# Optimization experiments

Measured on AMD Instinct MI355X. Metric: run time of the kernel, lower is better.

## Reference

```python
import jax, jax.numpy as jnp
import numpy as np

NODE_TYPES = ["patient", "visit", "symptom", "procedure", "disease", "drug"]
N = {"patient": 20000, "visit": 100000, "symptom": 4000, "procedure": 8000,
     "disease": 10000, "drug": 4000}
D = 128          # embedding_dim == hidden_channels
N_LAYERS = 4     # conv1..conv4
# (src, dst) per relation; reverse edges included so every node type gets messages
REL = [("patient", "visit"), ("visit", "patient"),
       ("visit", "symptom"), ("symptom", "visit"),
       ("visit", "procedure"), ("procedure", "visit"),
       ("visit", "disease"), ("disease", "visit"),
       ("visit", "drug"), ("drug", "visit")]
E_FWD = {("patient", "visit"): 100000, ("visit", "symptom"): 300000,
         ("visit", "procedure"): 200000, ("visit", "disease"): 250000,
         ("visit", "drug"): 300000}
EI_NAMES = ["ei_pv", "ei_vp", "ei_vs", "ei_sv", "ei_vpr", "ei_prv",
            "ei_vd", "ei_dv", "ei_vdr", "ei_drv"]
E_LABEL = 200000


def setup_inputs() -> dict:
    key = jax.random.key(0)
    ks = iter(jax.random.split(key, 64))
    inp = {}
    for nt in NODE_TYPES:
        inp[f"node_id_{nt}"] = jnp.arange(N[nt], dtype=jnp.int32)
        inp[f"emb_{nt}"] = jax.random.normal(next(ks), (N[nt], D), jnp.float32)
    for name, (src, dst) in zip(EI_NAMES, REL):
        e = E_FWD.get((src, dst), E_FWD.get((dst, src)))
        row = jax.random.randint(next(ks), (e,), 0, N[src], dtype=jnp.int32)
        col = jax.random.randint(next(ks), (e,), 0, N[dst], dtype=jnp.int32)
        inp[name] = jnp.stack([row, col])
    R = len(REL)
    inp["W_l"] = jax.random.normal(next(ks), (N_LAYERS, R, D, D), jnp.float32) * 0.05
    inp["b_l"] = jnp.zeros((N_LAYERS, R, D), jnp.float32)
    inp["W_r"] = jax.random.normal(next(ks), (N_LAYERS, R, D, D), jnp.float32) * 0.05
    inp["cls_w1"] = jax.random.normal(next(ks), (2 * D, D), jnp.float32) * 0.05
    inp["cls_b1"] = jnp.zeros((D,), jnp.float32)
    inp["cls_w2"] = jax.random.normal(next(ks), (D, 1), jnp.float32) * 0.05
    inp["cls_b2"] = jnp.zeros((1,), jnp.float32)
    row = jax.random.randint(next(ks), (E_LABEL,), 0, N["visit"], dtype=jnp.int32)
    col = jax.random.randint(next(ks), (E_LABEL,), 0, N["drug"], dtype=jnp.int32)
    inp["edge_label_index"] = jnp.stack([row, col])
    inp["edge_label"] = jax.random.bernoulli(next(ks), 0.5, (E_LABEL,)).astype(jnp.float32)
    return inp


def _hetero_sage_layer(x, eis, Wl, bl, Wr):
    # to_hetero semantics: out[dst] = sum over edge types (src,rel,dst) of
    #   SAGEConv_rel: lin_l(mean_j x[src][j]) + lin_r(x[dst])   (PyG defaults)
    out = {nt: jnp.zeros_like(v) for nt, v in x.items()}
    for r, (src, dst) in enumerate(REL):
        ei = eis[r]
        n_dst = x[dst].shape[0]
        msg = jax.ops.segment_sum(x[src][ei[0]], ei[1], num_segments=n_dst)
        deg = jax.ops.segment_sum(jnp.ones((ei.shape[1],), x[src].dtype), ei[1],
                                  num_segments=n_dst)
        mean = msg / jnp.maximum(deg, 1.0)[:, None]  # empty segments stay 0 as in PyG
        out[dst] = out[dst] + mean @ Wl[r] + bl[r] + x[dst] @ Wr[r]
    return out


def reference(node_id_patient, node_id_visit, node_id_symptom, node_id_procedure,
              node_id_disease, node_id_drug,
              emb_patient, emb_visit, emb_symptom, emb_procedure, emb_disease, emb_drug,
              ei_pv, ei_vp, ei_vs, ei_sv, ei_vpr, ei_prv, ei_vd, ei_dv, ei_vdr, ei_drv,
              W_l, b_l, W_r, cls_w1, cls_b1, cls_w2, cls_b2,
              edge_label_index, edge_label):
    x = {"patient": emb_patient[node_id_patient],
         "visit": emb_visit[node_id_visit],
         "symptom": emb_symptom[node_id_symptom],
         "procedure": emb_procedure[node_id_procedure],
         "disease": emb_disease[node_id_disease],
         "drug": emb_drug[node_id_drug]}
    eis = [ei_pv, ei_vp, ei_vs, ei_sv, ei_vpr, ei_prv, ei_vd, ei_dv, ei_vdr, ei_drv]
    for l in range(N_LAYERS):
        x = _hetero_sage_layer(x, eis, W_l[l], b_l[l], W_r[l])
        if l < N_LAYERS - 1:  # relu after conv1..conv3 only; dropout is eval-mode identity
            x = {k: jax.nn.relu(v) for k, v in x.items()}
    # Classifier: gather visit/drug node features per labeled edge, concat, MLP
    zv = x["visit"][edge_label_index[0]]
    zd = x["drug"][edge_label_index[1]]
    h = jax.nn.relu(jnp.concatenate([zv, zd], axis=-1) @ cls_w1 + cls_b1)
    pred = (h @ cls_w2 + cls_b2).reshape(-1)
    # BCE with logits: softplus(z) - z*y, mean-reduced
    loss = jnp.mean(jax.nn.softplus(pred) - pred * edge_label)
    return loss, pred
```

## Files before the change

kernel.cpp:

```cpp
#include <hip/hip_runtime.h>
#include <cmath>


typedef _Float16 f16x8 __attribute__((ext_vector_type(8)));
typedef float f32x4 __attribute__((ext_vector_type(4)));

#define NREL 10
#define NCOUNTS 546000
#define NEDGES  2300000
#define NVISIT  100000
#define NVEDGES 1150000
#define PLW 546816
#define WT_ELEMS (4 * PLW + 69632)
#define XELEMS 18688000UL
#define SELEMS 5888000UL
#define NBKT 873
#define BCAP 5056

struct GatherMeta { const float* emb[6]; const int* nid[6]; int rows[6]; int off[6]; };
struct BkMeta {
  const int* ei[NREL]; int E[NREL]; int cbc[NREL]; int ndst[NREL];
  int sh[NREL]; int bb[NREL]; int nb[NREL];
};
struct MTask {
  const _Float16* AH0; const _Float16* AL0;
  const _Float16* AH1; const _Float16* AL1;
  const _Float16* W;
  const float* bias;
  _Float16* outH; _Float16* outL;
  int M, blkOff, K, relu;
};
struct MMeta { MTask t[6]; int nTasks; };
struct F1Meta {
  const int* rp[5]; _Float16* mH[5]; _Float16* mL[5]; int aM[5]; int aOff[5];
  int nAgg; int aggTotal;
  const _Float16* gAH[5]; const _Float16* gAL[5]; const _Float16* gW[5];
  _Float16* gY[5]; int gM[5]; int gOff[5]; int nG;
};

__global__ __launch_bounds__(256) void conv0(GatherMeta g, _Float16* __restrict__ H,
                                             _Float16* __restrict__ L) {
  int t = blockIdx.y;
  int i = blockIdx.x * 256 + threadIdx.x;
  if (i >= g.rows[t] * 16) return;
  int row = i >> 4, q = i & 15;
  int s = g.nid[t][row];
  const float* p = g.emb[t] + (size_t)s * 128 + q * 8;
  float4 v0 = *(const float4*)p;
  float4 v1 = *(const float4*)(p + 4);
  float v[8] = {v0.x, v0.y, v0.z, v0.w, v1.x, v1.y, v1.z, v1.w};
  f16x8 h, l;
  #pragma unroll
  for (int j = 0; j < 8; ++j) {
    h[j] = (_Float16)v[j];
    l[j] = (_Float16)(v[j] - (float)h[j]);
  }
  size_t o = (size_t)(g.off[t] + row) * 128 + q * 8;
  *(f16x8*)(H + o) = h;
  *(f16x8*)(L + o) = l;
}

__global__ __launch_bounds__(256) void bkt_p1(BkMeta bm, int* __restrict__ bcur,
                                              int* __restrict__ bdata) {
  __shared__ int cnt[128];
  __shared__ int base[128];
  __shared__ unsigned short rnk[4096];
  int r = blockIdx.y;
  int E = bm.E[r], sh = bm.sh[r], bb = bm.bb[r], nb = bm.nb[r];
  int tid = threadIdx.x;
  if (tid < 128) cnt[tid] = 0;
  __syncthreads();
  int e0 = blockIdx.x * 4096;
  if (e0 >= E) return;
  const int* dstp = bm.ei[r] + E;
  const int* srcp = bm.ei[r];
  #pragma unroll
  for (int i = 0; i < 16; ++i) {
    int e = e0 + i * 256 + tid;
    if (e < E) {
      int b = dstp[e] >> sh;
      rnk[i * 256 + tid] = (unsigned short)atomicAdd(&cnt[b], 1);
    }
  }
  __syncthreads();
  if (tid < nb && cnt[tid] > 0) base[tid] = atomicAdd(&bcur[bb + tid], cnt[tid]);
  __syncthreads();
  #pragma unroll
  for (int i = 0; i < 16; ++i) {
    int e = e0 + i * 256 + tid;
    if (e < E) {
      int d = dstp[e];
      int b = d >> sh;
      int pos = base[b] + (int)rnk[i * 256 + tid];
      if (pos < BCAP)
        bdata[(size_t)(bb + b) * BCAP + pos] = ((d & ((1 << sh) - 1)) << 17) | srcp[e];
    }
  }
}

__global__ __launch_bounds__(256) void bkt_p2a(BkMeta bm, const int* __restrict__ bcur,
                                               const int* __restrict__ bdata,
                                               int* __restrict__ counts) {
  __shared__ int hist[2048];
  int g = blockIdx.x;
  int r = 0;
  #pragma unroll
  for (int i = 1; i < NREL; ++i) if (g >= bm.bb[i]) r = i;
  int lb = g - bm.bb[r];
  int sh = bm.sh[r], dpb = 1 << sh;
  int tid = threadIdx.x;
  for (int d = tid; d < dpb; d += 256) hist[d] = 0;
  __syncthreads();
  int cnt = bcur[g]; if (cnt > BCAP) cnt = BCAP;
  const int* bd = bdata + (size_t)g * BCAP;
  for (int i = tid; i < cnt; i += 256) atomicAdd(&hist[((unsigned)bd[i]) >> 17], 1);
  __syncthreads();
  int dBase = lb << sh;
  int dMax = bm.ndst[r] - dBase; if (dMax > dpb) dMax = dpb;
  for (int d = tid; d < dMax; d += 256) counts[bm.cbc[r] + dBase + d] = hist[d];
}

__global__ __launch_bounds__(1024) void scan1(const int* __restrict__ counts,
                                              int* __restrict__ partials) {
  __shared__ int s[1024];
  int i = blockIdx.x * 1024 + threadIdx.x;
  s[threadIdx.x] = (i < NCOUNTS) ? counts[i] : 0;
  __syncthreads();
  for (int off = 512; off > 0; off >>= 1) {
    if (threadIdx.x < off) s[threadIdx.x] += s[threadIdx.x + off];
    __syncthreads();
  }
  if (threadIdx.x == 0) partials[blockIdx.x] = s[0];
}

__global__ __launch_bounds__(1024) void scan2(int* __restrict__ partials, int nb) {
  __shared__ int s[1024];
  int t = threadIdx.x;
  int v = (t < nb) ? partials[t] : 0;
  s[t] = v;
  __syncthreads();
  for (int off = 1; off < 1024; off <<= 1) {
    int add = (t >= off) ? s[t - off] : 0;
    __syncthreads();
    s[t] += add;
    __syncthreads();
  }
  if (t < nb) partials[t] = s[t] - v;
}

__global__ __launch_bounds__(1024) void scan3(const int* __restrict__ counts,
                                              int* __restrict__ prefix,
                                              const int* __restrict__ partials) {
  __shared__ int s[1024];
  int t = threadIdx.x;
  int i = blockIdx.x * 1024 + t;
  int v = (i < NCOUNTS) ? counts[i] : 0;
  s[t] = v;
  __syncthreads();
  for (int off = 1; off < 1024; off <<= 1) {
    int add = (t >= off) ? s[t - off] : 0;
    __syncthreads();
    s[t] += add;
    __syncthreads();
  }
  int P = partials[blockIdx.x] + s[t] - v;
  if (i < NCOUNTS) prefix[i] = P;
  if (blockIdx.x == 0 && t == 0) prefix[NCOUNTS] = NEDGES;
}

__global__ __launch_bounds__(256) void bkt_p2b(BkMeta bm, const int* __restrict__ bcur,
                                               const int* __restrict__ bdata,
                                               const int* __restrict__ prefix,
                                               int* __restrict__ esrc) {
  __shared__ int pk[BCAP];
  __shared__ int srt[BCAP];
  __shared__ int cur[2048];
  __shared__ int part[256];
  __shared__ int baseSh;
  int g = blockIdx.x;
  int r = 0;
  #pragma unroll
  for (int i = 1; i < NREL; ++i) if (g >= bm.bb[i]) r = i;
  int lb = g - bm.bb[r];
  int sh = bm.sh[r], dpb = 1 << sh;
  int tid = threadIdx.x;
  int cnt = bcur[g]; if (cnt > BCAP) cnt = BCAP;
  const int* bd = bdata + (size_t)g * BCAP;
  for (int d = tid; d < dpb; d += 256) cur[d] = 0;
  for (int i = tid; i < cnt; i += 256) pk[i] = bd[i];
  __syncthreads();
  for (int i = tid; i < cnt; i += 256) atomicAdd(&cur[((unsigned)pk[i]) >> 17], 1);
  __syncthreads();
  int seg = (dpb + 255) >> 8;
  int s = 0;
  int b0 = tid * seg;
  for (int j = 0; j < seg; ++j) {
    int idx = b0 + j;
    if (idx < dpb) { int v = cur[idx]; cur[idx] = s; s += v; }
  }
  part[tid] = s;
  __syncthreads();
  for (int off = 1; off < 256; off <<= 1) {
    int add = (tid >= off) ? part[tid - off] : 0;
    __syncthreads();
    part[tid] += add;
    __syncthreads();
  }
  int myoff = part[tid] - s;
  for (int j = 0; j < seg; ++j) {
    int idx = b0 + j;
    if (idx < dpb) cur[idx] += myoff;
  }
  if (tid == 0) baseSh = prefix[bm.cbc[r] + (lb << sh)];
  __syncthreads();
  for (int i = tid; i < cnt; i += 256) {
    int p = pk[i];
    int pos = atomicAdd(&cur[((unsigned)p) >> 17], 1);
    srt[pos] = p & 0x1FFFF;
  }
  __syncthreads();
  int base = baseSh;
  for (int i = tid; i < cnt; i += 256) esrc[base + i] = srt[i];
}

__global__ __launch_bounds__(256) void merge_visit(const int* __restrict__ prefix,
                                                   const int* __restrict__ esrc,
                                                   int* __restrict__ mprefix,
                                                   int2* __restrict__ mesrc) {
  const int cbc[5]  = {0, 124000, 232000, 342000, 446000};
  const int yoff[5] = {0, 20000, 24000, 32000, 42000};
  int v = blockIdx.x * 256 + threadIdx.x;
  if (v >= NVISIT) return;
  int e0[5], e1[5];
  int base = 0;
  #pragma unroll
  for (int q = 0; q < 5; ++q) {
    e0[q] = prefix[cbc[q] + v];
    e1[q] = prefix[cbc[q] + v + 1];
    base += e0[q] - prefix[cbc[q]];
  }
  mprefix[v] = base;
  if (v == NVISIT - 1) {
    int t = base;
    #pragma unroll
    for (int q = 0; q < 5; ++q) t += e1[q] - e0[q];
    mprefix[NVISIT] = t;
  }
  int pos = base;
  #pragma unroll
  for (int q = 0; q < 5; ++q) {
    int d = e1[q] - e0[q];
    if (d > 0) {
      int wb = __float_as_int(1.f / (float)d);
      for (int e = e0[q]; e < e1[q]; ++e)
        mesrc[pos++] = make_int2(yoff[q] + esrc[e], wb);
    }
  }
}

__global__ __launch_bounds__(256) void prep_split(
    const float* __restrict__ W_l, const float* __restrict__ b_l,
    const float* __restrict__ W_r, const float* __restrict__ cw1,
    _Float16* __restrict__ Wt, float* __restrict__ visitSumB) {
  const int visitRel[5] = {0, 3, 5, 7, 9};
  const int inRel[5] = {1, 2, 4, 6, 8};
  int gid = blockIdx.x * 256 + threadIdx.x;
  if (gid < 1048576) {
    int l = gid >> 18, o = gid & 262143;
    float val; size_t base; int n, k, Kpad;
    if (o < 163840) {
      int t = o >> 15, e = o & 32767;
      k = e >> 7; n = e & 127; Kpad = 264;
      int r = inRel[t];
      val = (k < 128) ? W_l[(size_t)(l * 10 + r) * 16384 + k * 128 + n]
                      : W_r[(size_t)(l * 10 + r) * 16384 + (k - 128) * 128 + n];
      base = (size_t)l * PLW + t * 67584;
    } else if (o < 245760) {
      int q = (o - 163840) >> 14, e = (o - 163840) & 16383;
      k = e >> 7; n = e & 127; Kpad = 136;
      val = W_l[(size_t)(l * 10 + visitRel[q]) * 16384 + k * 128 + n];
      base = (size_t)l * PLW + 337920 + q * 34816;
    } else {
      int e = o - 245760;
      k = e >> 7; n = e & 127; Kpad = 136;
      val = 0.f;
      #pragma unroll
      for (int q = 0; q < 5; ++q)
        val += W_r[(size_t)(l * 10 + visitRel[q]) * 16384 + k * 128 + n];
      base = (size_t)l * PLW + 512000;
    }
    _Float16 h = (_Float16)val;
    _Float16 lo = (_Float16)(val - (float)h);
    Wt[base + (size_t)n * Kpad + k] = h;
    Wt[base + (size_t)(128 + n) * Kpad + k] = lo;
  } else if (gid < 1081344) {
    int e = gid - 1048576;
    int k = e >> 7, n = e & 127;
    float val = cw1[(size_t)k * 128 + n];
    _Float16 h = (_Float16)val;
    _Float16 lo = (_Float16)(val - (float)h);
    size_t base = (size_t)4 * PLW + (k < 128 ? 0 : 34816);
    int kk = k & 127;
    Wt[base + (size_t)n * 136 + kk] = h;
    Wt[base + (size_t)(128 + n) * 136 + kk] = lo;
  } else if (gid < 1081856) {
    int e = gid - 1081344;
    int l = e >> 7, c = e & 127;
    float val = 0.f;
    #pragma unroll
    for (int q = 0; q < 5; ++q) val += b_l[(l * 10 + visitRel[q]) * 128 + c];
    visitSumB[e] = val;
  }
}

__global__ __launch_bounds__(256, 8) void fused1(F1Meta f,
                                                 const _Float16* __restrict__ xvH,
                                                 const int* __restrict__ esrc) {
  int b = blockIdx.x;
  int tid = threadIdx.x;
  if (b < f.aggTotal) {
    int t = 0;
    #pragma unroll
    for (int i = 1; i < 5; ++i) if (i < f.nAgg && b >= f.aOff[i]) t = i;
    int row = (b - f.aOff[t]) * 16 + (tid >> 4);
    if (row >= f.aM[t]) return;
    int q = tid & 15;
    const int* rp = f.rp[t];
    int e0 = rp[row], e1 = rp[row + 1];
    float a[8];
    #pragma unroll
    for (int j = 0; j < 8; ++j) a[j] = 0.f;
    int e = e0;
    for (; e + 4 <= e1; e += 4) {
      int s0 = esrc[e], s1 = esrc[e + 1], s2 = esrc[e + 2], s3 = esrc[e + 3];
      f16x8 v0 = *(const f16x8*)(xvH + (size_t)s0 * 128 + q * 8);
      f16x8 v1 = *(const f16x8*)(xvH + (size_t)s1 * 128 + q * 8);
      f16x8 v2 = *(const f16x8*)(xvH + (size_t)s2 * 128 + q * 8);
      f16x8 v3 = *(const f16x8*)(xvH + (size_t)s3 * 128 + q * 8);
      #pragma unroll
      for (int j = 0; j < 8; ++j)
        a[j] += ((float)v0[j] + (float)v1[j]) + ((float)v2[j] + (float)v3[j]);
    }
    for (; e < e1; ++e) {
      int s = esrc[e];
      f16x8 v = *(const f16x8*)(xvH + (size_t)s * 128 + q * 8);
      #pragma unroll
      for (int j = 0; j < 8; ++j) a[j] += (float)v[j];
    }
    float inv = (e1 > e0) ? 1.f / (float)(e1 - e0) : 0.f;
    f16x8 h, l;
    #pragma unroll
    for (int j = 0; j < 8; ++j) {
      float v = a[j] * inv;
      h[j] = (_Float16)v;
      l[j] = (_Float16)(v - (float)h[j]);
    }
    size_t o = (size_t)row * 128 + q * 8;
    *(f16x8*)(f.mH[t] + o) = h;
    *(f16x8*)(f.mL[t] + o) = l;
    return;
  }
  b -= f.aggTotal;
  int g = 0;
  #pragma unroll
  for (int i = 1; i < 5; ++i) if (i < f.nG && b >= f.gOff[i]) g = i;
  int blockRow = (b - f.gOff[g]) * 32;
  int lane = tid & 63, wave = tid >> 6;
  int quad = lane >> 4, lm = lane & 15;
  int wr = wave >> 1, wc = wave & 1;
  const _Float16* AH = f.gAH[g];
  const _Float16* AL = f.gAL[g];
  const _Float16* W = f.gW[g];
  int M = f.gM[g];
  int ar = blockRow + wr * 16 + lm;
  if (ar >= M) ar = M - 1;
  f32x4 acc[4];
  #pragma unroll
  for (int nt = 0; nt < 4; ++nt) acc[nt] = (f32x4){0.f, 0.f, 0.f, 0.f};
  for (int ks = 0; ks < 128; ks += 32) {
    f16x8 ah = *(const f16x8*)(AH + (size_t)ar * 128 + ks + quad * 8);
    f16x8 al = *(const f16x8*)(AL + (size_t)ar * 128 + ks + quad * 8);
    #pragma unroll
    for (int nt = 0; nt < 4; ++nt) {
      int n = wc * 64 + nt * 16 + lm;
      f16x8 bh = *(const f16x8*)(W + (size_t)n * 136 + ks + quad * 8);
      f16x8 bl = *(const f16x8*)(W + (size_t)(128 + n) * 136 + ks + quad * 8);
      acc[nt] = __builtin_amdgcn_mfma_f32_16x16x32_f16(ah, bh, acc[nt], 0, 0, 0);
      acc[nt] = __builtin_amdgcn_mfma_f32_16x16x32_f16(ah, bl, acc[nt], 0, 0, 0);
      acc[nt] = __builtin_amdgcn_mfma_f32_16x16x32_f16(al, bh, acc[nt], 0, 0, 0);
    }
  }
  _Float16* Y = f.gY[g];
  #pragma unroll
  for (int i = 0; i < 4; ++i) {
    int grow = blockRow + wr * 16 + quad * 4 + i;
    if (grow >= M) continue;
    #pragma unroll
    for (int nt = 0; nt < 4; ++nt)
      Y[(size_t)grow * 128 + wc * 64 + nt * 16 + lm] = (_Float16)acc[nt][i];
  }
}

__global__ __launch_bounds__(256) void agg_visit(const int* __restrict__ mprefix,
                                                 const int2* __restrict__ mesrc,
                                                 const _Float16* __restrict__ YH,
                                                 _Float16* __restrict__ xvH,
                                                 _Float16* __restrict__ xvL, int doRelu) {
  int row = blockIdx.x * 16 + (threadIdx.x >> 4);
  if (row >= NVISIT) return;
  int q = threadIdx.x & 15;
  size_t o = (size_t)row * 128 + q * 8;
  f16x8 h0 = *(f16x8*)(xvH + o);
  f16x8 l0 = *(f16x8*)(xvL + o);
  float a[8];
  #pragma unroll
  for (int j = 0; j < 8; ++j) a[j] = (float)h0[j] + (float)l0[j];
  int e0 = mprefix[row], e1 = mprefix[row + 1];
  int e = e0;
  for (; e + 4 <= e1; e += 4) {
    int2 p0 = mesrc[e], p1 = mesrc[e + 1], p2 = mesrc[e + 2], p3 = mesrc[e + 3];
    f16x8 v0 = *(const f16x8*)(YH + (size_t)p0.x * 128 + q * 8);
    f16x8 v1 = *(const f16x8*)(YH + (size_t)p1.x * 128 + q * 8);
    f16x8 v2 = *(const f16x8*)(YH + (size_t)p2.x * 128 + q * 8);
    f16x8 v3 = *(const f16x8*)(YH + (size_t)p3.x * 128 + q * 8);
    float w0 = __int_as_float(p0.y), w1 = __int_as_float(p1.y);
    float w2 = __int_as_float(p2.y), w3 = __int_as_float(p3.y);
    #pragma unroll
    for (int j = 0; j < 8; ++j)
      a[j] += (w0 * (float)v0[j] + w1 * (float)v1[j]) +
              (w2 * (float)v2[j] + w3 * (float)v3[j]);
  }
  for (; e < e1; ++e) {
    int2 p = mesrc[e];
    f16x8 v = *(const f16x8*)(YH + (size_t)p.x * 128 + q * 8);
    float w = __int_as_float(p.y);
    #pragma unroll
    for (int j = 0; j < 8; ++j) a[j] += w * (float)v[j];
  }
  f16x8 h, l;
  #pragma unroll
  for (int j = 0; j < 8; ++j) {
    float v = doRelu ? fmaxf(a[j], 0.f) : a[j];
    h[j] = (_Float16)v;
    l[j] = (_Float16)(v - (float)h[j]);
  }
  *(f16x8*)(xvH + o) = h;
  *(f16x8*)(xvL + o) = l;
}

__global__ __launch_bounds__(256, 2) void mgemm(MMeta mm) {
  int b = blockIdx.x;
  int ti = 0;
  for (int i = 1; i < mm.nTasks; ++i) if (b >= mm.t[i].blkOff) ti = i;
  MTask tk = mm.t[ti];
  int blockRow = (b - tk.blkOff) * 128;
  int Kpad = tk.K + 8;

  __shared__ _Float16 Ash[2][128][72];
  int tid = threadIdx.x;
  int wave = tid >> 6, lane = tid & 63;
  int quad = lane >> 4, lm = lane & 15;
  int wr = wave >> 1, wc = wave & 1;

  f32x4 acc[4][4];
  #pragma unroll
  for (int i = 0; i < 4; ++i)
    #pragma unroll
    for (int j = 0; j < 4; ++j) acc[i][j] = (f32x4){0.f, 0.f, 0.f, 0.f};

  const _Float16* wrowH[4];
  const _Float16* wrowL[4];
  #pragma unroll
  for (int nt = 0; nt < 4; ++nt) {
    int n = wc * 64 + nt * 16 + lm;
    wrowH[nt] = tk.W + (size_t)n * Kpad;
    wrowL[nt] = tk.W + (size_t)(128 + n) * Kpad;
  }

  int sr = tid >> 1, sk = (tid & 1) * 32;
  int gr = blockRow + sr; if (gr >= tk.M) gr = tk.M - 1;
  for (int k0 = 0; k0 < tk.K; k0 += 64) {
    const _Float16* AH = (k0 < 128) ? tk.AH0 : tk.AH1;
    const _Float16* AL = (k0 < 128) ? tk.AL0 : tk.AL1;
    size_t abase = (size_t)gr * 128 + (k0 & 127) + sk;
    #pragma unroll
    for (int c = 0; c < 4; ++c) {
      *(f16x8*)&Ash[0][sr][sk + c * 8] = *(const f16x8*)(AH + abase + c * 8);
      *(f16x8*)&Ash[1][sr][sk + c * 8] = *(const f16x8*)(AL + abase + c * 8);
    }
    __syncthreads();
    #pragma unroll
    for (int ks = 0; ks < 64; ks += 32) {
      int kf = k0 + ks + quad * 8;
      f16x8 bh[4], bl[4];
      #pragma unroll
      for (int nt = 0; nt < 4; ++nt) {
        bh[nt] = *(const f16x8*)(wrowH[nt] + kf);
        bl[nt] = *(const f16x8*)(wrowL[nt] + kf);
      }
      #pragma unroll
      for (int mt = 0; mt < 4; ++mt) {
        int r = wr * 64 + mt * 16 + lm;
        f16x8 ah = *(const f16x8*)&Ash[0][r][ks + quad * 8];
        f16x8 al = *(const f16x8*)&Ash[1][r][ks + quad * 8];
        #pragma unroll
        for (int nt = 0; nt < 4; ++nt) {
          acc[mt][nt] = __builtin_amdgcn_mfma_f32_16x16x32_f16(ah, bh[nt], acc[mt][nt], 0, 0, 0);
          acc[mt][nt] = __builtin_amdgcn_mfma_f32_16x16x32_f16(ah, bl[nt], acc[mt][nt], 0, 0, 0);
          acc[mt][nt] = __builtin_amdgcn_mfma_f32_16x16x32_f16(al, bh[nt], acc[mt][nt], 0, 0, 0);
        }
      }
    }
    __syncthreads();
  }

  float bv[4];
  #pragma unroll
  for (int nt = 0; nt < 4; ++nt)
    bv[nt] = tk.bias ? tk.bias[wc * 64 + nt * 16 + lm] : 0.f;
  #pragma unroll
  for (int mt = 0; mt < 4; ++mt) {
    #pragma unroll
    for (int i = 0; i < 4; ++i) {
      int grow = blockRow + wr * 64 + mt * 16 + quad * 4 + i;
      if (grow >= tk.M) continue;
      size_t ob = (size_t)grow * 128 + wc * 64 + lm;
      #pragma unroll
      for (int nt = 0; nt < 4; ++nt) {
        float v = acc[mt][nt][i] + bv[nt];
        if (tk.relu) v = fmaxf(v, 0.f);
        _Float16 h = (_Float16)v;
        tk.outH[ob + nt * 16] = h;
        if (tk.outL) tk.outL[ob + nt * 16] = (_Float16)(v - (float)h);
      }
    }
  }
}

__global__ __launch_bounds__(256) void cls_edge(
    const _Float16* __restrict__ UH, const _Float16* __restrict__ UL,
    const _Float16* __restrict__ VH, const _Float16* __restrict__ VL,
    const int* __restrict__ eli, const float* __restrict__ w2,
    const float* __restrict__ b2, const float* __restrict__ y,
    float* __restrict__ lossOut, float* __restrict__ pred, int M) {
  __shared__ float lsum[4];
  int tid = threadIdx.x;
  int q = tid & 15;
  int lane = tid & 63;
  float w2v[8];
  #pragma unroll
  for (int j = 0; j < 8; ++j) w2v[j] = w2[q * 8 + j];
  float bias = b2[0];
  float lacc = 0.f;
  int e0 = blockIdx.x * 128 + (tid >> 4);
  #pragma unroll
  for (int p = 0; p < 8; ++p) {
    int e = e0 + p * 16;
    if (e < M) {
      int vi = eli[e], di = eli[M + e];
      size_t uo = (size_t)vi * 128 + q * 8;
      size_t vo = (size_t)di * 128 + q * 8;
      f16x8 uh = *(const f16x8*)(UH + uo);
      f16x8 ul = *(const f16x8*)(UL + uo);
      f16x8 vh = *(const f16x8*)(VH + vo);
      f16x8 vl = *(const f16x8*)(VL + vo);
      float part = 0.f;
      #pragma unroll
      for (int j = 0; j < 8; ++j) {
        float t = ((float)uh[j] + (float)ul[j]) + ((float)vh[j] + (float)vl[j]);
        part += fmaxf(t, 0.f) * w2v[j];
      }
      part += __shfl_xor(part, 1);
      part += __shfl_xor(part, 2);
      part += __shfl_xor(part, 4);
      part += __shfl_xor(part, 8);
      if (q == 0) {
        float z = part + bias;
        pred[e] = z;
        lacc += fmaxf(z, 0.f) + log1pf(expf(-fabsf(z))) - z * y[e];
      }
    }
  }
  lacc += __shfl_xor(lacc, 16);
  lacc += __shfl_xor(lacc, 32);
  if (lane == 0) lsum[tid >> 6] = lacc;
  __syncthreads();
  if (tid == 0)
    atomicAdd(lossOut, (lsum[0] + lsum[1] + lsum[2] + lsum[3]) * (1.0f / 200000.0f));
}

extern "C" void kernel_launch(void* const* d_in, const int* in_sizes, int n_in,
                              void* d_out, int out_size, void* d_ws, size_t ws_size,
                              hipStream_t stream) {
  static const int kRows[6] = {20000, 100000, 4000, 8000, 10000, 4000};
  static const int kOff[6]  = {0, 20000, 120000, 124000, 132000, 142000};
  static const int kSmallT[5]   = {0, 2, 3, 4, 5};
  static const int kInRel[5]    = {1, 2, 4, 6, 8};
  static const int kCbcIn[5]    = {100000, 120000, 224000, 332000, 442000};
  static const int kYOff[5]     = {0, 20000, 24000, 32000, 42000};
  static const int kBOff[5]     = {0, 157, 189, 252, 331};
  static const int kAggOff[5]   = {0, 1250, 1500, 2000, 2625};
  static const int kLeanOff[5]  = {0, 625, 750, 1000, 1313};
  const int kAggTotal = 2875, kLeanTotal = 1438;
  static const int kCbcA[NREL]  = {0, 100000, 120000, 124000, 224000,
                                   232000, 332000, 342000, 442000, 446000};
  static const int kEhA[NREL]   = {100000, 100000, 300000, 300000, 200000,
                                   200000, 250000, 250000, 300000, 300000};
  static const int kNdst[NREL]  = {100000, 20000, 4000, 100000, 8000,
                                   100000, 10000, 100000, 4000, 100000};
  static const int kSh[NREL]    = {11, 9, 5, 10, 7, 10, 7, 10, 5, 10};
  static const int kNB[NREL]    = {49, 40, 125, 98, 63, 98, 79, 98, 125, 98};
  static const int kBB[NREL]    = {0, 49, 89, 214, 312, 375, 473, 552, 650, 775};

  const float* W_l = (const float*)d_in[22];
  const float* b_l = (const float*)d_in[23];
  const float* W_r = (const float*)d_in[24];
  const float* cw1 = (const float*)d_in[25];
  const float* cb1 = (const float*)d_in[26];
  const float* cw2 = (const float*)d_in[27];
  const float* cb2 = (const float*)d_in[28];
  const int* eli = (const int*)d_in[29];
  const float* ylab = (const float*)d_in[30];

  _Float16* H = (_Float16*)d_ws;
  _Float16* L = H + XELEMS;
  _Float16* meanH = L + XELEMS;
  _Float16* meanL = meanH + SELEMS;
  _Float16* YH = meanL + SELEMS;
  _Float16* Wt = YH + SELEMS;
  int* prefix = (int*)(Wt + WT_ELEMS);
  int* counts = prefix + 546004;
  int* esrc = counts + NCOUNTS;
  int* partials = esrc + NEDGES;
  float* visitSumB = (float*)(partials + 1024);
  int* bcur = (int*)(visitSumB + 512);
  int* bdata = bcur + 1024;

  int* mprefix = counts;
  int2* mesrc = (int2*)bdata;

  _Float16* UH = meanH;
  _Float16* VH = meanH + (size_t)NVISIT * 128;
  _Float16* VL = VH + (size_t)4000 * 128;
  _Float16* UL = (_Float16*)prefix;

  BkMeta bm;
  for (int r = 0; r < NREL; ++r) {
    bm.ei[r] = (const int*)d_in[12 + r];
    bm.E[r] = kEhA[r];
    bm.cbc[r] = kCbcA[r];
    bm.ndst[r] = kNdst[r];
    bm.sh[r] = kSh[r];
    bm.bb[r] = kBB[r];
    bm.nb[r] = kNB[r];
  }

  hipMemsetAsync(bcur, 0, NBKT * sizeof(int), stream);
  hipMemsetAsync(d_out, 0, sizeof(float), stream);

  prep_split<<<(1081856 + 255) / 256, 256, 0, stream>>>(W_l, b_l, W_r, cw1, Wt, visitSumB);

  GatherMeta gm;
  for (int t = 0; t < 6; ++t) {
    gm.nid[t] = (const int*)d_in[2 * t];
    gm.emb[t] = (const float*)d_in[2 * t + 1];
    gm.rows[t] = kRows[t];
    gm.off[t] = kOff[t];
  }
  conv0<<<dim3(6250, 6), 256, 0, stream>>>(gm, H, L);

  bkt_p1<<<dim3(74, NREL), 256, 0, stream>>>(bm, bcur, bdata);
  bkt_p2a<<<dim3(NBKT), 256, 0, stream>>>(bm, bcur, bdata, counts);
  scan1<<<534, 1024, 0, stream>>>(counts, partials);
  scan2<<<1, 1024, 0, stream>>>(partials, 534);
  scan3<<<534, 1024, 0, stream>>>(counts, prefix, partials);
  bkt_p2b<<<dim3(NBKT), 256, 0, stream>>>(bm, bcur, bdata, prefix, esrc);
  merge_visit<<<dim3((NVISIT + 255) / 256), 256, 0, stream>>>(prefix, esrc, mprefix, mesrc);

  _Float16* xvH = H + (size_t)kOff[1] * 128;
  _Float16* xvL = L + (size_t)kOff[1] * 128;

  for (int l = 0; l < 4; ++l) {
    int doRelu = (l < 3);
    int last = (l == 3);
    _Float16* LW = Wt + (size_t)l * PLW;

    F1Meta f1;
    if (!last) {
      for (int t = 0; t < 5; ++t) {
        f1.rp[t] = prefix + kCbcIn[t];
        f1.mH[t] = meanH + (size_t)kYOff[t] * 128;
        f1.mL[t] = meanL + (size_t)kYOff[t] * 128;
        f1.aM[t] = kRows[kSmallT[t]];
        f1.aOff[t] = kAggOff[t];
      }
      f1.nAgg = 5;
      f1.aggTotal = kAggTotal;
    } else {
      f1.rp[0] = prefix + kCbcIn[4];
      f1.mH[0] = meanH + (size_t)kYOff[4] * 128;
      f1.mL[0] = meanL + (size_t)kYOff[4] * 128;
      f1.aM[0] = 4000;
      f1.aOff[0] = 0;
      for (int t = 1; t < 5; ++t) { f1.rp[t] = nullptr; f1.mH[t] = nullptr; f1.mL[t] = nullptr; f1.aM[t] = 0; f1.aOff[t] = 0; }
      f1.nAgg = 1;
      f1.aggTotal = 250;
    }
    for (int q = 0; q < 5; ++q) {
      size_t so = (size_t)kOff[kSmallT[q]] * 128;
      f1.gAH[q] = H + so;
      f1.gAL[q] = L + so;
      f1.gW[q] = LW + 337920 + (size_t)q * 34816;
      f1.gY[q] = YH + (size_t)kYOff[q] * 128;
      f1.gM[q] = kRows[kSmallT[q]];
      f1.gOff[q] = kLeanOff[q];
    }
    f1.nG = 5;
    fused1<<<dim3(f1.aggTotal + kLeanTotal), 256, 0, stream>>>(f1, xvH, esrc);

    MMeta m;
    if (!last) {
      m.nTasks = 6;
      for (int t = 0; t < 5; ++t) {
        size_t mo = (size_t)kYOff[t] * 128;
        size_t so = (size_t)kOff[kSmallT[t]] * 128;
        m.t[t].AH0 = meanH + mo; m.t[t].AL0 = meanL + mo;
        m.t[t].AH1 = H + so;     m.t[t].AL1 = L + so;
        m.t[t].W = LW + (size_t)t * 67584;
        m.t[t].bias = b_l + (size_t)(l * 10 + kInRel[t]) * 128;
        m.t[t].outH = H + so;    m.t[t].outL = L + so;
        m.t[t].M = kRows[kSmallT[t]];
        m.t[t].blkOff = kBOff[t];
        m.t[t].K = 256;
        m.t[t].relu = doRelu;
      }
      m.t[5].AH0 = xvH; m.t[5].AL0 = xvL;
      m.t[5].AH1 = nullptr; m.t[5].AL1 = nullptr;
      m.t[5].W = LW + 512000;
      m.t[5].bias = visitSumB + l * 128;
      m.t[5].outH = xvH; m.t[5].outL = xvL;
      m.t[5].M = NVISIT;
      m.t[5].blkOff = 363;
      m.t[5].K = 128;
      m.t[5].relu = 0;
      mgemm<<<dim3(363 + 782), 256, 0, stream>>>(m);
    } else {
      size_t mo = (size_t)kYOff[4] * 128;
      size_t so = (size_t)kOff[5] * 128;
      m.nTasks = 2;
      m.t[0].AH0 = meanH + mo; m.t[0].AL0 = meanL + mo;
      m.t[0].AH1 = H + so;     m.t[0].AL1 = L + so;
      m.t[0].W = LW + (size_t)4 * 67584;
      m.t[0].bias = b_l + (size_t)(l * 10 + kInRel[4]) * 128;
      m.t[0].outH = H + so;    m.t[0].outL = L + so;
      m.t[0].M = 4000;
      m.t[0].blkOff = 0;
      m.t[0].K = 256;
      m.t[0].relu = 0;
      m.t[1].AH0 = xvH; m.t[1].AL0 = xvL;
      m.t[1].AH1 = nullptr; m.t[1].AL1 = nullptr;
      m.t[1].W = LW + 512000;
      m.t[1].bias = visitSumB + l * 128;
      m.t[1].outH = xvH; m.t[1].outL = xvL;
      m.t[1].M = NVISIT;
      m.t[1].blkOff = 32;
      m.t[1].K = 128;
      m.t[1].relu = 0;
      mgemm<<<dim3(32 + 782), 256, 0, stream>>>(m);
    }

    agg_visit<<<dim3(6250), 256, 0, stream>>>(mprefix, mesrc, YH, xvH, xvL, doRelu);
  }

  MMeta muv;
  muv.nTasks = 2;
  muv.t[0].AH0 = xvH; muv.t[0].AL0 = xvL;
  muv.t[0].AH1 = nullptr; muv.t[0].AL1 = nullptr;
  muv.t[0].W = Wt + (size_t)4 * PLW;
  muv.t[0].bias = cb1;
  muv.t[0].outH = UH; muv.t[0].outL = UL;
  muv.t[0].M = NVISIT;
  muv.t[0].blkOff = 0;
  muv.t[0].K = 128;
  muv.t[0].relu = 0;
  muv.t[1].AH0 = H + (size_t)kOff[5] * 128; muv.t[1].AL0 = L + (size_t)kOff[5] * 128;
  muv.t[1].AH1 = nullptr; muv.t[1].AL1 = nullptr;
  muv.t[1].W = Wt + (size_t)4 * PLW + 34816;
  muv.t[1].bias = nullptr;
  muv.t[1].outH = VH; muv.t[1].outL = VL;
  muv.t[1].M = 4000;
  muv.t[1].blkOff = 782;
  muv.t[1].K = 128;
  muv.t[1].relu = 0;
  mgemm<<<dim3(782 + 32), 256, 0, stream>>>(muv);

  const int ML = 200000;
  cls_edge<<<dim3((ML + 127) / 128), 256, 0, stream>>>(
      UH, UL, VH, VL, eli, cw2, cb2, ylab,
      (float*)d_out, (float*)d_out + 1, ML);
}
```

Measured before the change: 911.0 us.

## Move small-type SAGE GEMMs into visit aggregation kernel and reorder fused1 blocks

The update GEMMs for the small node types move out of the mgemm launch into a new fused3 kernel, where they run alongside the visit-row aggregation blocks. mgemm now handles only the visit self-GEMM. In fused1, the lean GEMM blocks are placed before the aggregation blocks so the MFMA-heavy work is dispatched first. The goal is to overlap compute-bound small GEMMs with the memory-bound visit gather and to cut load imbalance across launches. In exchange, fused3 uses a hardcoded 264 weight stride and adds a __syncthreads inside the GEMM branch.

```diff
diff --git a/kernel.cpp b/kernel.cpp
--- a/kernel.cpp
+++ b/kernel.cpp
@@ -32,10 +32,15 @@
 };
 struct MMeta { MTask t[6]; int nTasks; };
 struct F1Meta {
-  const int* rp[5]; _Float16* mH[5]; _Float16* mL[5]; int aM[5]; int aOff[5];
-  int nAgg; int aggTotal;
+  const int* rp[5]; _Float16* mH[5]; _Float16* mL[5]; int aM[5]; int aOff[5]; int nAgg;
   const _Float16* gAH[5]; const _Float16* gAL[5]; const _Float16* gW[5];
-  _Float16* gY[5]; int gM[5]; int gOff[5]; int nG;
+  _Float16* gY[5]; int gM[5]; int gOff[5]; int nG; int leanTotal;
+};
+struct F3Meta {
+  const _Float16* mMH[5]; const _Float16* mML[5];
+  _Float16* mXH[5]; _Float16* mXL[5];
+  const _Float16* mW[5]; const float* mB[5];
+  int mM[5]; int mOff[5]; int nM1; int m1Total;
 };
 
 __global__ __launch_bounds__(256) void conv0(GatherMeta g, _Float16* __restrict__ H,
@@ -318,97 +323,157 @@
                                                  const int* __restrict__ esrc) {
   int b = blockIdx.x;
   int tid = threadIdx.x;
-  if (b < f.aggTotal) {
-    int t = 0;
-    #pragma unroll
-    for (int i = 1; i < 5; ++i) if (i < f.nAgg && b >= f.aOff[i]) t = i;
-    int row = (b - f.aOff[t]) * 16 + (tid >> 4);
-    if (row >= f.aM[t]) return;
-    int q = tid & 15;
-    const int* rp = f.rp[t];
-    int e0 = rp[row], e1 = rp[row + 1];
-    float a[8];
-    #pragma unroll
-    for (int j = 0; j < 8; ++j) a[j] = 0.f;
-    int e = e0;
-    for (; e + 4 <= e1; e += 4) {
-      int s0 = esrc[e], s1 = esrc[e + 1], s2 = esrc[e + 2], s3 = esrc[e + 3];
-      f16x8 v0 = *(const f16x8*)(xvH + (size_t)s0 * 128 + q * 8);
-      f16x8 v1 = *(const f16x8*)(xvH + (size_t)s1 * 128 + q * 8);
-      f16x8 v2 = *(const f16x8*)(xvH + (size_t)s2 * 128 + q * 8);
-      f16x8 v3 = *(const f16x8*)(xvH + (size_t)s3 * 128 + q * 8);
+  if (b < f.leanTotal) {
+    int g = 0;
+    #pragma unroll
+    for (int i = 1; i < 5; ++i) if (i < f.nG && b >= f.gOff[i]) g = i;
+    int blockRow = (b - f.gOff[g]) * 32;
+    int lane = tid & 63, wave = tid >> 6;
+    int quad = lane >> 4, lm = lane & 15;
+    int wr = wave >> 1, wc = wave & 1;
+    const _Float16* AH = f.gAH[g];
+    const _Float16* AL = f.gAL[g];
+    const _Float16* W = f.gW[g];
+    int M = f.gM[g];
+    int ar = blockRow + wr * 16 + lm;
+    if (ar >= M) ar = M - 1;
+    f32x4 acc[4];
+    #pragma unroll
+    for (int nt = 0; nt < 4; ++nt) acc[nt] = (f32x4){0.f, 0.f, 0.f, 0.f};
+    for (int ks = 0; ks < 128; ks += 32) {
+      f16x8 ah = *(const f16x8*)(AH + (size_t)ar * 128 + ks + quad * 8);
+      f16x8 al = *(const f16x8*)(AL + (size_t)ar * 128 + ks + quad * 8);
       #pragma unroll
-      for (int j = 0; j < 8; ++j)
-        a[j] += ((float)v0[j] + (float)v1[j]) + ((float)v2[j] + (float)v3[j]);
-    }
-    for (; e < e1; ++e) {
-      int s = esrc[e];
-      f16x8 v = *(const f16x8*)(xvH + (size_t)s * 128 + q * 8);
+      for (int nt = 0; nt < 4; ++nt) {
+        int n = wc * 64 + nt * 16 + lm;
+        f16x8 bh = *(const f16x8*)(W + (size_t)n * 136 + ks + quad * 8);
+        f16x8 bl = *(const f16x8*)(W + (size_t)(128 + n) * 136 + ks + quad * 8);
+        acc[nt] = __builtin_amdgcn_mfma_f32_16x16x32_f16(ah, bh, acc[nt], 0, 0, 0);
+        acc[nt] = __builtin_amdgcn_mfma_f32_16x16x32_f16(ah, bl, acc[nt], 0, 0, 0);
+        acc[nt] = __builtin_amdgcn_mfma_f32_16x16x32_f16(al, bh, acc[nt], 0, 0, 0);
+      }
+    }
+    _Float16* Y = f.gY[g];
+    #pragma unroll
+    for (int i = 0; i < 4; ++i) {
+      int grow = blockRow + wr * 16 + quad * 4 + i;
+      if (grow >= M) continue;
       #pragma unroll
-      for (int j = 0; j < 8; ++j) a[j] += (float)v[j];
-    }
-    float inv = (e1 > e0) ? 1.f / (float)(e1 - e0) : 0.f;
-    f16x8 h, l;
-    #pragma unroll
-    for (int j = 0; j < 8; ++j) {
-      float v = a[j] * inv;
-      h[j] = (_Float16)v;
-      l[j] = (_Float16)(v - (float)h[j]);
-    }
-    size_t o = (size_t)row * 128 + q * 8;
-    *(f16x8*)(f.mH[t] + o) = h;
-    *(f16x8*)(f.mL[t] + o) = l;
+      for (int nt = 0; nt < 4; ++nt)
+        Y[(size_t)grow * 128 + wc * 64 + nt * 16 + lm] = (_Float16)acc[nt][i];
+    }
     return;
   }
-  b -= f.aggTotal;
-  int g = 0;
-  #pragma unroll
-  for (int i = 1; i < 5; ++i) if (i < f.nG && b >= f.gOff[i]) g = i;
-  int blockRow = (b - f.gOff[g]) * 32;
-  int lane = tid & 63, wave = tid >> 6;
-  int quad = lane >> 4, lm = lane & 15;
-  int wr = wave >> 1, wc = wave & 1;
-  const _Float16* AH = f.gAH[g];
-  const _Float16* AL = f.gAL[g];
-  const _Float16* W = f.gW[g];
-  int M = f.gM[g];
-  int ar = blockRow + wr * 16 + lm;
-  if (ar >= M) ar = M - 1;
-  f32x4 acc[4];
-  #pragma unroll
-  for (int nt = 0; nt < 4; ++nt) acc[nt] = (f32x4){0.f, 0.f, 0.f, 0.f};
-  for (int ks = 0; ks < 128; ks += 32) {
-    f16x8 ah = *(const f16x8*)(AH + (size_t)ar * 128 + ks + quad * 8);
-    f16x8 al = *(const f16x8*)(AL + (size_t)ar * 128 + ks + quad * 8);
-    #pragma unroll
-    for (int nt = 0; nt < 4; ++nt) {
-      int n = wc * 64 + nt * 16 + lm;
-      f16x8 bh = *(const f16x8*)(W + (size_t)n * 136 + ks + quad * 8);
-      f16x8 bl = *(const f16x8*)(W + (size_t)(128 + n) * 136 + ks + quad * 8);
-      acc[nt] = __builtin_amdgcn_mfma_f32_16x16x32_f16(ah, bh, acc[nt], 0, 0, 0);
-      acc[nt] = __builtin_amdgcn_mfma_f32_16x16x32_f16(ah, bl, acc[nt], 0, 0, 0);
-      acc[nt] = __builtin_amdgcn_mfma_f32_16x16x32_f16(al, bh, acc[nt], 0, 0, 0);
-    }
-  }
-  _Float16* Y = f.gY[g];
-  #pragma unroll
-  for (int i = 0; i < 4; ++i) {
-    int grow = blockRow + wr * 16 + quad * 4 + i;
-    if (grow >= M) continue;
-    #pragma unroll
-    for (int nt = 0; nt < 4; ++nt)
-      Y[(size_t)grow * 128 + wc * 64 + nt * 16 + lm] = (_Float16)acc[nt][i];
-  }
-}
-
-__global__ __launch_bounds__(256) void agg_visit(const int* __restrict__ mprefix,
+  b -= f.leanTotal;
+  int t = 0;
+  #pragma unroll
+  for (int i = 1; i < 5; ++i) if (i < f.nAgg && b >= f.aOff[i]) t = i;
+  int row = (b - f.aOff[t]) * 16 + (tid >> 4);
+  if (row >= f.aM[t]) return;
+  int q = tid & 15;
+  const int* rp = f.rp[t];
+  int e0 = rp[row], e1 = rp[row + 1];
+  float a[8];
+  #pragma unroll
+  for (int j = 0; j < 8; ++j) a[j] = 0.f;
+  int e = e0;
+  for (; e + 4 <= e1; e += 4) {
+    int s0 = esrc[e], s1 = esrc[e + 1], s2 = esrc[e + 2], s3 = esrc[e + 3];
+    f16x8 v0 = *(const f16x8*)(xvH + (size_t)s0 * 128 + q * 8);
+    f16x8 v1 = *(const f16x8*)(xvH + (size_t)s1 * 128 + q * 8);
+    f16x8 v2 = *(const f16x8*)(xvH + (size_t)s2 * 128 + q * 8);
+    f16x8 v3 = *(const f16x8*)(xvH + (size_t)s3 * 128 + q * 8);
+    #pragma unroll
+    for (int j = 0; j < 8; ++j)
+      a[j] += ((float)v0[j] + (float)v1[j]) + ((float)v2[j] + (float)v3[j]);
+  }
+  for (; e < e1; ++e) {
+    int s = esrc[e];
+    f16x8 v = *(const f16x8*)(xvH + (size_t)s * 128 + q * 8);
+    #pragma unroll
+    for (int j = 0; j < 8; ++j) a[j] += (float)v[j];
+  }
+  float inv = (e1 > e0) ? 1.f / (float)(e1 - e0) : 0.f;
+  f16x8 h, l;
+  #pragma unroll
+  for (int j = 0; j < 8; ++j) {
+    float v = a[j] * inv;
+    h[j] = (_Float16)v;
+    l[j] = (_Float16)(v - (float)h[j]);
+  }
+  size_t o = (size_t)row * 128 + q * 8;
+  *(f16x8*)(f.mH[t] + o) = h;
+  *(f16x8*)(f.mL[t] + o) = l;
+}
+
+__global__ __launch_bounds__(256, 8) void fused3(F3Meta f,
+                                                 const int* __restrict__ mprefix,
                                                  const int2* __restrict__ mesrc,
                                                  const _Float16* __restrict__ YH,
                                                  _Float16* __restrict__ xvH,
-                                                 _Float16* __restrict__ xvL, int doRelu) {
-  int row = blockIdx.x * 16 + (threadIdx.x >> 4);
+                                                 _Float16* __restrict__ xvL,
+                                                 int doRelu) {
+  int b = blockIdx.x;
+  int tid = threadIdx.x;
+  if (b < f.m1Total) {
+    int g = 0;
+    #pragma unroll
+    for (int i = 1; i < 5; ++i) if (i < f.nM1 && b >= f.mOff[i]) g = i;
+    int blockRow = (b - f.mOff[g]) * 32;
+    int lane = tid & 63, wave = tid >> 6;
+    int quad = lane >> 4, lm = lane & 15;
+    int wr = wave >> 1, wc = wave & 1;
+    int M = f.mM[g];
+    int ar = blockRow + wr * 16 + lm;
+    if (ar >= M) ar = M - 1;
+    const _Float16* MH = f.mMH[g];
+    const _Float16* ML = f.mML[g];
+    _Float16* XH = f.mXH[g];
+    _Float16* XL = f.mXL[g];
+    const _Float16* W = f.mW[g];
+    f32x4 acc[4];
+    #pragma unroll
+    for (int nt = 0; nt < 4; ++nt) acc[nt] = (f32x4){0.f, 0.f, 0.f, 0.f};
+    for (int ks = 0; ks < 256; ks += 32) {
+      const _Float16* AH = (ks < 128) ? MH : (const _Float16*)XH;
+      const _Float16* AL = (ks < 128) ? ML : (const _Float16*)XL;
+      int kk = ks & 127;
+      f16x8 ah = *(const f16x8*)(AH + (size_t)ar * 128 + kk + quad * 8);
+      f16x8 al = *(const f16x8*)(AL + (size_t)ar * 128 + kk + quad * 8);
+      #pragma unroll
+      for (int nt = 0; nt < 4; ++nt) {
+        int n = wc * 64 + nt * 16 + lm;
+        f16x8 bh = *(const f16x8*)(W + (size_t)n * 264 + ks + quad * 8);
+        f16x8 bl = *(const f16x8*)(W + (size_t)(128 + n) * 264 + ks + quad * 8);
+        acc[nt] = __builtin_amdgcn_mfma_f32_16x16x32_f16(ah, bh, acc[nt], 0, 0, 0);
+        acc[nt] = __builtin_amdgcn_mfma_f32_16x16x32_f16(ah, bl, acc[nt], 0, 0, 0);
+        acc[nt] = __builtin_amdgcn_mfma_f32_16x16x32_f16(al, bh, acc[nt], 0, 0, 0);
+      }
+    }
+    __syncthreads();
+    float bv[4];
+    #pragma unroll
+    for (int nt = 0; nt < 4; ++nt) bv[nt] = f.mB[g][wc * 64 + nt * 16 + lm];
+    #pragma unroll
+    for (int i = 0; i < 4; ++i) {
+      int grow = blockRow + wr * 16 + quad * 4 + i;
+      if (grow >= M) continue;
+      size_t ob = (size_t)grow * 128 + wc * 64 + lm;
+      #pragma unroll
+      for (int nt = 0; nt < 4; ++nt) {
+        float v = acc[nt][i] + bv[nt];
+        if (doRelu) v = fmaxf(v, 0.f);
+        _Float16 h = (_Float16)v;
+        XH[ob + nt * 16] = h;
+        XL[ob + nt * 16] = (_Float16)(v - (float)h);
+      }
+    }
+    return;
+  }
+  b -= f.m1Total;
+  int row = b * 16 + (tid >> 4);
   if (row >= NVISIT) return;
-  int q = threadIdx.x & 15;
+  int q = tid & 15;
   size_t o = (size_t)row * 128 + q * 8;
   f16x8 h0 = *(f16x8*)(xvH + o);
   f16x8 l0 = *(f16x8*)(xvL + o);
@@ -598,7 +663,6 @@
   static const int kInRel[5]    = {1, 2, 4, 6, 8};
   static const int kCbcIn[5]    = {100000, 120000, 224000, 332000, 442000};
   static const int kYOff[5]     = {0, 20000, 24000, 32000, 42000};
-  static const int kBOff[5]     = {0, 157, 189, 252, 331};
   static const int kAggOff[5]   = {0, 1250, 1500, 2000, 2625};
   static const int kLeanOff[5]  = {0, 625, 750, 1000, 1313};
   const int kAggTotal = 2875, kLeanTotal = 1438;
@@ -686,6 +750,18 @@
     _Float16* LW = Wt + (size_t)l * PLW;
 
     F1Meta f1;
+    f1.leanTotal = kLeanTotal;
+    for (int q = 0; q < 5; ++q) {
+      size_t so = (size_t)kOff[kSmallT[q]] * 128;
+      f1.gAH[q] = H + so;
+      f1.gAL[q] = L + so;
+      f1.gW[q] = LW + 337920 + (size_t)q * 34816;
+      f1.gY[q] = YH + (size_t)kYOff[q] * 128;
+      f1.gM[q] = kRows[kSmallT[q]];
+      f1.gOff[q] = kLeanOff[q];
+    }
+    f1.nG = 5;
+    int aggTotal;
     if (!last) {
       for (int t = 0; t < 5; ++t) {
         f1.rp[t] = prefix + kCbcIn[t];
@@ -695,7 +771,7 @@
         f1.aOff[t] = kAggOff[t];
       }
       f1.nAgg = 5;
-      f1.aggTotal = kAggTotal;
+      aggTotal = kAggTotal;
     } else {
       f1.rp[0] = prefix + kCbcIn[4];
       f1.mH[0] = meanH + (size_t)kYOff[4] * 128;
@@ -704,72 +780,51 @@
       f1.aOff[0] = 0;
       for (int t = 1; t < 5; ++t) { f1.rp[t] = nullptr; f1.mH[t] = nullptr; f1.mL[t] = nullptr; f1.aM[t] = 0; f1.aOff[t] = 0; }
       f1.nAgg = 1;
-      f1.aggTotal = 250;
-    }
-    for (int q = 0; q < 5; ++q) {
-      size_t so = (size_t)kOff[kSmallT[q]] * 128;
-      f1.gAH[q] = H + so;
-      f1.gAL[q] = L + so;
-      f1.gW[q] = LW + 337920 + (size_t)q * 34816;
-      f1.gY[q] = YH + (size_t)kYOff[q] * 128;
-      f1.gM[q] = kRows[kSmallT[q]];
-      f1.gOff[q] = kLeanOff[q];
-    }
-    f1.nG = 5;
-    fused1<<<dim3(f1.aggTotal + kLeanTotal), 256, 0, stream>>>(f1, xvH, esrc);
+      aggTotal = 250;
+    }
+    fused1<<<dim3(kLeanTotal + aggTotal), 256, 0, stream>>>(f1, xvH, esrc);
 
     MMeta m;
+    m.nTasks = 1;
+    m.t[0].AH0 = xvH; m.t[0].AL0 = xvL;
+    m.t[0].AH1 = nullptr; m.t[0].AL1 = nullptr;
+    m.t[0].W = LW + 512000;
+    m.t[0].bias = visitSumB + l * 128;
+    m.t[0].outH = xvH; m.t[0].outL = xvL;
+    m.t[0].M = NVISIT;
+    m.t[0].blkOff = 0;
+    m.t[0].K = 128;
+    m.t[0].relu = 0;
+    mgemm<<<dim3(782), 256, 0, stream>>>(m);
+
+    F3Meta f3;
     if (!last) {
-      m.nTasks = 6;
       for (int t = 0; t < 5; ++t) {
         size_t mo = (size_t)kYOff[t] * 128;
         size_t so = (size_t)kOff[kSmallT[t]] * 128;
-        m.t[t].AH0 = meanH + mo; m.t[t].AL0 = meanL + mo;
-        m.t[t].AH1 = H + so;     m.t[t].AL1 = L + so;
-        m.t[t].W = LW + (size_t)t * 67584;
-        m.t[t].bias = b_l + (size_t)(l * 10 + kInRel[t]) * 128;
-        m.t[t].outH = H + so;    m.t[t].outL = L + so;
-        m.t[t].M = kRows[kSmallT[t]];
-        m.t[t].blkOff = kBOff[t];
-        m.t[t].K = 256;
-        m.t[t].relu = doRelu;
-      }
-      m.t[5].AH0 = xvH; m.t[5].AL0 = xvL;
-      m.t[5].AH1 = nullptr; m.t[5].AL1 = nullptr;
-      m.t[5].W = LW + 512000;
-      m.t[5].bias = visitSumB + l * 128;
-      m.t[5].outH = xvH; m.t[5].outL = xvL;
-      m.t[5].M = NVISIT;
-      m.t[5].blkOff = 363;
-      m.t[5].K = 128;
-      m.t[5].relu = 0;
-      mgemm<<<dim3(363 + 782), 256, 0, stream>>>(m);
+        f3.mMH[t] = meanH + mo; f3.mML[t] = meanL + mo;
+        f3.mXH[t] = H + so;     f3.mXL[t] = L + so;
+        f3.mW[t] = LW + (size_t)t * 67584;
+        f3.mB[t] = b_l + (size_t)(l * 10 + kInRel[t]) * 128;
+        f3.mM[t] = kRows[kSmallT[t]];
+        f3.mOff[t] = kLeanOff[t];
+      }
+      f3.nM1 = 5;
+      f3.m1Total = kLeanTotal;
     } else {
       size_t mo = (size_t)kYOff[4] * 128;
       size_t so = (size_t)kOff[5] * 128;
-      m.nTasks = 2;
-      m.t[0].AH0 = meanH + mo; m.t[0].AL0 = meanL + mo;
-      m.t[0].AH1 = H + so;     m.t[0].AL1 = L + so;
-      m.t[0].W = LW + (size_t)4 * 67584;
-      m.t[0].bias = b_l + (size_t)(l * 10 + kInRel[4]) * 128;
-      m.t[0].outH = H + so;    m.t[0].outL = L + so;
-      m.t[0].M = 4000;
-      m.t[0].blkOff = 0;
-      m.t[0].K = 256;
-      m.t[0].relu = 0;
-      m.t[1].AH0 = xvH; m.t[1].AL0 = xvL;
-      m.t[1].AH1 = nullptr; m.t[1].AL1 = nullptr;
-      m.t[1].W = LW + 512000;
-      m.t[1].bias = visitSumB + l * 128;
-      m.t[1].outH = xvH; m.t[1].outL = xvL;
-      m.t[1].M = NVISIT;
-      m.t[1].blkOff = 32;
-      m.t[1].K = 128;
-      m.t[1].relu = 0;
-      mgemm<<<dim3(32 + 782), 256, 0, stream>>>(m);
-    }
-
-    agg_visit<<<dim3(6250), 256, 0, stream>>>(mprefix, mesrc, YH, xvH, xvL, doRelu);
+      f3.mMH[0] = meanH + mo; f3.mML[0] = meanL + mo;
+      f3.mXH[0] = H + so;     f3.mXL[0] = L + so;
+      f3.mW[0] = LW + (size_t)4 * 67584;
+      f3.mB[0] = b_l + (size_t)(l * 10 + kInRel[4]) * 128;
+      f3.mM[0] = 4000;
+      f3.mOff[0] = 0;
+      for (int t = 1; t < 5; ++t) { f3.mMH[t] = nullptr; f3.mML[t] = nullptr; f3.mXH[t] = nullptr; f3.mXL[t] = nullptr; f3.mW[t] = nullptr; f3.mB[t] = nullptr; f3.mM[t] = 0; f3.mOff[t] = 0; }
+      f3.nM1 = 1;
+      f3.m1Total = 125;
+    }
+    fused3<<<dim3(f3.m1Total + 6250), 256, 0, stream>>>(f3, mprefix, mesrc, YH, xvH, xvL, doRelu);
   }
 
   MMeta muv;
```

After: 987.2 us. 8.4% more time.
